# Kernel tuning notes

Measured on AMD Instinct MI355X. Metric: run time of the kernel, lower is better.

Reference implementation:

```python
import jax, jax.numpy as jnp
import numpy as np

N, L, D, PD, H, C, NP = 4, 512, 128, 64, 8, 32, 8  # batch, len, node_dim, pair_dim, heads, hidden, points
INF = 1e5
EPS = 1e-5


def _ln(x, g, b):
    m = jnp.mean(x, -1, keepdims=True)
    v = jnp.mean((x - m) ** 2, -1, keepdims=True)
    return (x - m) * jax.lax.rsqrt(v + EPS) * g + b


def _local_to_global(R, t, p):
    # p: (N,L,...,3); global = R @ p + t
    out = jnp.einsum('nlij,nl...j->nl...i', R, p)
    t_b = t.reshape(t.shape[0], t.shape[1], *([1] * (p.ndim - 3)), 3)
    return out + t_b


def _global_to_local(R, t, q):
    # local = R^T @ (q - t)
    t_b = t.reshape(t.shape[0], t.shape[1], *([1] * (q.ndim - 3)), 3)
    return jnp.einsum('nlij,nl...i->nl...j', R, q - t_b)


def _alpha_from_logits(logits, mask):
    # logits (N,L,L,H), mask (N,L,L) bool over key dim
    m = mask[..., None]
    lg = jnp.where(m, logits, logits - INF)
    a = jax.nn.softmax(lg, axis=2)
    return jnp.where(m, a, jnp.zeros_like(a))


def setup_inputs() -> dict:
    key = jax.random.key(0)
    ks = jax.random.split(key, 24)
    s = 0.02
    inp = {
        'R': jax.random.normal(ks[0], (N, L, 3, 3), jnp.float32),
        't': jax.random.normal(ks[1], (N, L, 3), jnp.float32),
        'x': jax.random.normal(ks[2], (N, L, D), jnp.float32),
        'z': jax.random.normal(ks[3], (N, L, L, PD), jnp.float32),
        'intra_mask': jax.random.bernoulli(ks[4], 0.5, (N, L, L)),
        'inter_mask': jax.random.bernoulli(ks[5], 0.5, (N, L, L)),
        'Wq': jax.random.normal(ks[6], (D, H * C), jnp.float32) * s,
        'Wk': jax.random.normal(ks[7], (D, H * C), jnp.float32) * s,
        'Wv': jax.random.normal(ks[8], (D, H * C), jnp.float32) * s,
        'Wpair': jax.random.normal(ks[9], (PD, H), jnp.float32) * s,
        'spatial_coef': jnp.full((1, 1, 1, H), np.log(np.exp(1.0) - 1.0), jnp.float32),
        'Wqp': jax.random.normal(ks[10], (D, NP * H * 3), jnp.float32) * s,
        'Wkp': jax.random.normal(ks[11], (D, NP * H * 3), jnp.float32) * s,
        'Wvp': jax.random.normal(ks[12], (D, NP * H * 3), jnp.float32) * s,
        'W1': jax.random.normal(ks[13], (H * PD + H * C + H * NP, D), jnp.float32) * s,
        'b1': jnp.zeros((D,), jnp.float32),
        'W2a': jax.random.normal(ks[14], (D, D), jnp.float32) * s,
        'b2a': jnp.zeros((D,), jnp.float32),
        'W2b': jax.random.normal(ks[15], (D, D), jnp.float32) * s,
        'b2b': jnp.zeros((D,), jnp.float32),
        'W2c': jax.random.normal(ks[16], (D, D), jnp.float32) * s,
        'b2c': jnp.zeros((D,), jnp.float32),
        'ln1_g': jnp.ones((D,), jnp.float32),
        'ln1_b': jnp.zeros((D,), jnp.float32),
        'ln2_g': jnp.ones((D,), jnp.float32),
        'ln2_b': jnp.zeros((D,), jnp.float32),
    }
    return inp


def _forward(R, t, x, z, intra_mask, inter_mask, Wq, Wk, Wv, Wpair, spatial_coef,
             Wqp, Wkp, Wvp, W1, b1, W2a, b2a, W2b, b2b, W2c, b2c,
             ln1_g, ln1_b, ln2_g, ln2_b):
    # ---- attention logits ----
    qn = (x @ Wq).reshape(N, L, H, C)
    kn = (x @ Wk).reshape(N, L, H, C)
    logits_node = jnp.einsum('nlhc,nmhc->nlmh', qn, kn) * (1.0 / np.sqrt(C))
    logits_pair = z @ Wpair  # (N,L,L,H)
    qp = _local_to_global(R, t, (x @ Wqp).reshape(N, L, H * NP, 3)).reshape(N, L, H, NP * 3)
    kp = _local_to_global(R, t, (x @ Wkp).reshape(N, L, H * NP, 3)).reshape(N, L, H, NP * 3)
    # ||q-k||^2 expanded to avoid (N,L,L,H,3P) intermediate
    sum_sq = ((qp ** 2).sum(-1)[:, :, None, :]
              + ((kp ** 2).sum(-1))[:, None, :, :]
              - 2.0 * jnp.einsum('nlhc,nmhc->nlmh', qp, kp))
    gamma = jax.nn.softplus(spatial_coef)  # (1,1,1,H)
    logits_spatial = sum_sq * (-gamma * np.sqrt(2.0 / (9.0 * NP)) / 2.0)
    logits = (logits_node + logits_pair + logits_spatial) * np.sqrt(1.0 / 3.0)

    # ---- dual-mask softmax blend ----
    intra_s = intra_mask.sum((-1, -2)).astype(jnp.float32)
    inter_s = inter_mask.sum((-1, -2)).astype(jnp.float32)
    ratio = (intra_s / (intra_s + inter_s))[:, None, None, None]
    alpha = (_alpha_from_logits(logits, intra_mask) * ratio
             + _alpha_from_logits(logits, inter_mask) * (1.0 - ratio))

    # ---- 3-stream aggregation ----
    vn = (x @ Wv).reshape(N, L, H, C)
    feat_node = jnp.einsum('nlmh,nmhc->nlhc', alpha, vn).reshape(N, L, H * C)
    feat_pair = jnp.einsum('nlmh,nlmp->nlhp', alpha, z).reshape(N, L, H * PD)
    vp = _local_to_global(R, t, (x @ Wvp).reshape(N, L, H * NP, 3)).reshape(N, L, H, NP, 3)
    fs = jnp.einsum('nlmh,nmhpc->nlhpc', alpha, vp)  # (N,L,H,P,3)
    fs = _global_to_local(R, t, fs)
    feat_spatial = jnp.linalg.norm(fs, axis=-1).reshape(N, L, H * NP)
    agg = jnp.concatenate([feat_node, feat_pair, feat_spatial], axis=-1)

    # ---- transitions ----
    feats = _ln(x + agg @ W1 + b1, ln1_g, ln1_b)
    h = jax.nn.relu(feats @ W2a + b2a)
    h = jax.nn.relu(h @ W2b + b2b)
    out = h @ W2c + b2c
    # codebook_head == 1 -> residual branch
    return _ln(feats + out, ln2_g, ln2_b)


def reference(R, t, x, z, intra_mask, inter_mask, Wq, Wk, Wv, Wpair, spatial_coef,
              Wqp, Wkp, Wvp, W1, b1, W2a, b2a, W2b, b2b, W2c, b2c,
              ln1_g, ln1_b, ln2_g, ln2_b):
    return _forward(R, t, x, z, intra_mask, inter_mask, Wq, Wk, Wv, Wpair, spatial_coef,
                    Wqp, Wkp, Wvp, W1, b1, W2a, b2a, W2b, b2b, W2c, b2c,
                    ln1_g, ln1_b, ln2_g, ln2_b)
```

## Files before the change

### kernel.cpp

```cpp
#include <hip/hip_runtime.h>
#include <math.h>

constexpr int kN = 4, kL = 512, kD = 128, kPD = 64, kH = 8, kC = 32, kNP = 8;

constexpr long OFF_FLAG = 0;
constexpr long OFF_RATIO = 16;
constexpr long OFF_SUMS = 24;
constexpr long OFF_QN  = 32;
constexpr long OFF_KN  = OFF_QN  + (long)kN * kL * 256;
constexpr long OFF_VN  = OFF_KN  + (long)kN * kL * 256;
constexpr long OFF_QP  = OFF_VN  + (long)kN * kL * 256;
constexpr long OFF_KP  = OFF_QP  + (long)kN * kL * 192;
constexpr long OFF_VP  = OFF_KP  + (long)kN * kL * 192;
constexpr long OFF_QP2 = OFF_VP  + (long)kN * kL * 192;
constexpr long OFF_KP2 = OFF_QP2 + (long)kN * kL * 8;
constexpr long OFF_AGG = OFF_KP2 + (long)kN * kL * 8;

__device__ __forceinline__ bool mask_at(const void* p, long idx, int mt) {
  if (mt == 0) return ((const unsigned char*)p)[idx] != 0;
  if (mt == 1) return ((const int*)p)[idx] != 0;
  return ((const float*)p)[idx] != 0.0f;
}

__global__ __launch_bounds__(256) void detect_mask_type_kernel(
    const unsigned int* __restrict__ m, int* __restrict__ flag) {
  __shared__ int sFloat, sGt1;
  if (threadIdx.x == 0) { sFloat = 0; sGt1 = 0; }
  __syncthreads();
  int isFloat = 0, gt1 = 0;
#pragma unroll
  for (int i = 0; i < 4; ++i) {
    const unsigned int w = m[threadIdx.x + i * 256];
    if (w == 0x3F800000u) isFloat = 1;
    if (w > 1u) gt1 = 1;
  }
  if (isFloat) atomicOr(&sFloat, 1);
  if (gt1) atomicOr(&sGt1, 1);
  __syncthreads();
  if (threadIdx.x == 0) {
    *flag = sFloat ? 2 : (sGt1 ? 0 : 1);
  }
}

__global__ void zero_sums_kernel(float* __restrict__ sums) {
  if (threadIdx.x < 8) sums[threadIdx.x] = 0.f;
}

__global__ __launch_bounds__(256) void mask_ratio_partial_kernel(
    const void* __restrict__ intra, const void* __restrict__ inter,
    const int* __restrict__ flag, float* __restrict__ sums) {
  __shared__ float red[2][256];
  const int tid = threadIdx.x;
  const int bid = blockIdx.x;
  const int n = bid >> 6;
  const int mt = *flag;
  const long base = (long)n * kL * kL + (long)(bid & 63) * 4096;
  float si = 0.f, st = 0.f;
  for (int i = tid; i < 4096; i += 256) {
    si += mask_at(intra, base + i, mt) ? 1.f : 0.f;
    st += mask_at(inter, base + i, mt) ? 1.f : 0.f;
  }
  red[0][tid] = si; red[1][tid] = st;
  __syncthreads();
  for (int s = 128; s > 0; s >>= 1) {
    if (tid < s) { red[0][tid] += red[0][tid + s]; red[1][tid] += red[1][tid + s]; }
    __syncthreads();
  }
  if (tid == 0) {
    atomicAdd(&sums[n * 2 + 0], red[0][0]);
    atomicAdd(&sums[n * 2 + 1], red[1][0]);
  }
}

__global__ void mask_ratio_final_kernel(const float* __restrict__ sums,
                                        float* __restrict__ ratio) {
  const int n = threadIdx.x;
  if (n < kN) ratio[n] = sums[n * 2] / (sums[n * 2] + sums[n * 2 + 1]);
}

__global__ __launch_bounds__(256) void proj_kernel(
    const float* __restrict__ x, const float* __restrict__ R,
    const float* __restrict__ t,
    const float* __restrict__ Wq, const float* __restrict__ Wk,
    const float* __restrict__ Wv, const float* __restrict__ Wqp,
    const float* __restrict__ Wkp, const float* __restrict__ Wvp,
    float* __restrict__ qn, float* __restrict__ kn, float* __restrict__ vn,
    float* __restrict__ qp, float* __restrict__ kp, float* __restrict__ vp,
    float* __restrict__ qp2, float* __restrict__ kp2) {
  __shared__ float xs[8][128];
  __shared__ float plocal[8][192];
  __shared__ float pglob[8][192];
  __shared__ float Rl[8][9];
  __shared__ float tl[8][3];
  const int tid = threadIdx.x;
  const int bid = blockIdx.x;
  const int n = bid >> 6;
  const int l0 = (bid & 63) * 8;
  const long rowbase = (long)n * kL + l0;

  for (int f = tid * 4; f < 8 * 128; f += 256 * 4) {
    const float4 v = *(const float4*)&x[rowbase * 128 + f];
    *(float4*)&xs[f >> 7][f & 127] = v;
  }
  if (tid < 72) Rl[tid / 9][tid % 9] = R[rowbase * 9 + tid];
  if (tid >= 72 && tid < 96) { int q = tid - 72; tl[q / 3][q % 3] = t[rowbase * 3 + q]; }
  __syncthreads();

  {
    const float* Ws[3] = {Wq, Wk, Wv};
    float* Os[3] = {qn, kn, vn};
    for (int wmat = 0; wmat < 3; ++wmat) {
      const float* W = Ws[wmat];
      float acc[8];
#pragma unroll
      for (int r = 0; r < 8; ++r) acc[r] = 0.f;
      for (int k = 0; k < 128; ++k) {
        const float w = W[k * 256 + tid];
#pragma unroll
        for (int r = 0; r < 8; ++r) acc[r] = fmaf(xs[r][k], w, acc[r]);
      }
#pragma unroll
      for (int r = 0; r < 8; ++r) Os[wmat][(rowbase + r) * 256 + tid] = acc[r];
    }
  }

  {
    const float* Ws[3] = {Wqp, Wkp, Wvp};
    float* Os[3] = {qp, kp, vp};
    float* O2s[2] = {qp2, kp2};
    for (int wmat = 0; wmat < 3; ++wmat) {
      __syncthreads();
      if (tid < 192) {
        const float* W = Ws[wmat];
        float acc[8];
#pragma unroll
        for (int r = 0; r < 8; ++r) acc[r] = 0.f;
        for (int k = 0; k < 128; ++k) {
          const float w = W[k * 192 + tid];
#pragma unroll
          for (int r = 0; r < 8; ++r) acc[r] = fmaf(xs[r][k], w, acc[r]);
        }
#pragma unroll
        for (int r = 0; r < 8; ++r) plocal[r][tid] = acc[r];
      }
      __syncthreads();
      for (int task = tid; task < 512; task += 256) {
        const int r = task >> 6, hp = task & 63;
        const float px = plocal[r][hp * 3 + 0];
        const float py = plocal[r][hp * 3 + 1];
        const float pz = plocal[r][hp * 3 + 2];
#pragma unroll
        for (int i = 0; i < 3; ++i) {
          const float g = Rl[r][i * 3 + 0] * px + Rl[r][i * 3 + 1] * py +
                          Rl[r][i * 3 + 2] * pz + tl[r][i];
          pglob[r][hp * 3 + i] = g;
          Os[wmat][(rowbase + r) * 192 + hp * 3 + i] = g;
        }
      }
      __syncthreads();
      if (wmat < 2 && tid < 64) {
        const int r = tid >> 3, h = tid & 7;
        float s = 0.f;
#pragma unroll
        for (int j = 0; j < 24; ++j) {
          const float v = pglob[r][h * 24 + j];
          s = fmaf(v, v, s);
        }
        O2s[wmat][(rowbase + r) * 8 + h] = s;
      }
    }
  }
}

__global__ __launch_bounds__(256) void attn_kernel(
    const float* __restrict__ z, const void* __restrict__ intra,
    const void* __restrict__ inter, const int* __restrict__ flag,
    const float* __restrict__ ratio_arr,
    const float* __restrict__ R, const float* __restrict__ t,
    const float* __restrict__ qn, const float* __restrict__ kn,
    const float* __restrict__ vn, const float* __restrict__ qp,
    const float* __restrict__ kp, const float* __restrict__ vp,
    const float* __restrict__ qp2, const float* __restrict__ kp2,
    const float* __restrict__ Wpair, const float* __restrict__ spatial_coef,
    float* __restrict__ agg) {
  __shared__ float lg[512][8];
  __shared__ float zbuf[64][68];
  __shared__ float mI[512], mT[512];
  __shared__ float qn_l[8][36];
  __shared__ float qp_l[192];
  __shared__ float wp[64][8];
  __shared__ float red[2][256];
  __shared__ float smax[2][8], rmul[2][8];
  __shared__ float qp2_l[8], coef_l[8];
  __shared__ float fsbuf[192];
  __shared__ float Rl[9], tl[3];

  const int tid = threadIdx.x;
  const int bid = blockIdx.x;
  const int n = bid >> 9, l = bid & 511;
  const long row = (long)n * kL + l;
  const long nbase = (long)n * kL;
  const int mt = *flag;
  const float ratio = ratio_arr[n];

  qn_l[tid >> 5][tid & 31] = qn[row * 256 + tid];
  if (tid < 192) qp_l[tid] = qp[row * 192 + tid];
  if (tid < 8) {
    qp2_l[tid] = qp2[row * 8 + tid];
    const float g = logf(1.f + expf(spatial_coef[tid]));
    coef_l[tid] = -g * sqrtf(2.f / (9.f * kNP)) * 0.5f;
  }
  for (int i = tid; i < 512; i += 256) wp[i >> 3][i & 7] = Wpair[i];
  if (tid < 9) Rl[tid] = R[row * 9 + tid];
  if (tid >= 16 && tid < 19) tl[tid - 16] = t[row * 3 + (tid - 16)];
  {
    const long mbase = row * kL;
    for (int m = tid; m < 512; m += 256) {
      mI[m] = mask_at(intra, mbase + m, mt) ? 1.f : 0.f;
      mT[m] = mask_at(inter, mbase + m, mt) ? 1.f : 0.f;
    }
  }
  __syncthreads();

  const float invsC = 0.17677669529663687f;
  const float invs3 = 0.5773502691896258f;
  const int h = tid & 7, m0 = tid >> 3;
  const float coef = coef_l[h];
  const float q2h = qp2_l[h];

  for (int mc = 0; mc < 8; ++mc) {
    __syncthreads();
    {
      const float* zrow = z + (row * kL + mc * 64) * 64;
      for (int f = tid * 4; f < 4096; f += 1024)
        *(float4*)&zbuf[f >> 6][f & 63] = *(const float4*)&zrow[f];
    }
    __syncthreads();
#pragma unroll
    for (int half = 0; half < 2; ++half) {
      const int mm = m0 + half * 32;
      const int mg = mc * 64 + mm;
      float dn = 0.f;
      const float* knp = &kn[(nbase + mg) * 256 + h * 32];
#pragma unroll
      for (int c4 = 0; c4 < 8; ++c4) {
        const float4 kv = *(const float4*)&knp[c4 * 4];
        dn = fmaf(qn_l[h][c4 * 4 + 0], kv.x, dn);
        dn = fmaf(qn_l[h][c4 * 4 + 1], kv.y, dn);
        dn = fmaf(qn_l[h][c4 * 4 + 2], kv.z, dn);
        dn = fmaf(qn_l[h][c4 * 4 + 3], kv.w, dn);
      }
      float dp = 0.f;
#pragma unroll 16
      for (int p = 0; p < 64; ++p) dp = fmaf(wp[p][h], zbuf[mm][p], dp);
      float ds = 0.f;
      const float* kpp = &kp[(nbase + mg) * 192 + h * 24];
      const float* qpp = &qp_l[h * 24];
#pragma unroll
      for (int j4 = 0; j4 < 6; ++j4) {
        const float4 kv = *(const float4*)&kpp[j4 * 4];
        ds = fmaf(qpp[j4 * 4 + 0], kv.x, ds);
        ds = fmaf(qpp[j4 * 4 + 1], kv.y, ds);
        ds = fmaf(qpp[j4 * 4 + 2], kv.z, ds);
        ds = fmaf(qpp[j4 * 4 + 3], kv.w, ds);
      }
      const float sumsq = q2h + kp2[(nbase + mg) * 8 + h] - 2.f * ds;
      lg[mg][h] = (dn * invsC + dp + sumsq * coef) * invs3;
    }
  }
  __syncthreads();

  const int h2 = tid & 7, j = tid >> 3;
  float mxI = -3.0e38f, mxT = -3.0e38f;
  for (int m = j; m < 512; m += 32) {
    const float v = lg[m][h2];
    if (mI[m] != 0.f && v > mxI) mxI = v;
    if (mT[m] != 0.f && v > mxT) mxT = v;
  }
  red[0][tid] = mxI; red[1][tid] = mxT;
  __syncthreads();
  for (int s = 16; s > 0; s >>= 1) {
    if (j < s) {
      red[0][tid] = fmaxf(red[0][tid], red[0][tid + s * 8]);
      red[1][tid] = fmaxf(red[1][tid], red[1][tid + s * 8]);
    }
    __syncthreads();
  }
  if (tid < 8) { smax[0][tid] = red[0][tid]; smax[1][tid] = red[1][tid]; }
  __syncthreads();
  const float mxIh = smax[0][h2], mxTh = smax[1][h2];
  float suI = 0.f, suT = 0.f;
  for (int m = j; m < 512; m += 32) {
    const float v = lg[m][h2];
    if (mI[m] != 0.f) suI += expf(v - mxIh);
    if (mT[m] != 0.f) suT += expf(v - mxTh);
  }
  red[0][tid] = suI; red[1][tid] = suT;
  __syncthreads();
  for (int s = 16; s > 0; s >>= 1) {
    if (j < s) {
      red[0][tid] += red[0][tid + s * 8];
      red[1][tid] += red[1][tid + s * 8];
    }
    __syncthreads();
  }
  if (tid < 8) {
    rmul[0][tid] = ratio / red[0][tid];
    rmul[1][tid] = (1.f - ratio) / red[1][tid];
  }
  __syncthreads();
  for (int idx = tid; idx < 4096; idx += 256) {
    const int m = idx >> 3, hh = idx & 7;
    const float v = lg[m][hh];
    float a = 0.f;
    if (mI[m] != 0.f) a = expf(v - smax[0][hh]) * rmul[0][hh];
    if (mT[m] != 0.f) a += expf(v - smax[1][hh]) * rmul[1][hh];
    lg[m][hh] = a;
  }
  __syncthreads();

  const int hn = tid >> 5;
  const int po = tid * 2;
  const int hpair = po >> 6, pp = po & 63;
  const int hs = tid / 24;
  float accN = 0.f, accP0 = 0.f, accP1 = 0.f, accS = 0.f;
  for (int mc = 0; mc < 8; ++mc) {
    __syncthreads();
    {
      const float* zrow = z + (row * kL + mc * 64) * 64;
      for (int f = tid * 4; f < 4096; f += 1024)
        *(float4*)&zbuf[f >> 6][f & 63] = *(const float4*)&zrow[f];
    }
    __syncthreads();
#pragma unroll 4
    for (int mm = 0; mm < 64; ++mm) {
      const int mg = mc * 64 + mm;
      const float aN = lg[mg][hn];
      accN = fmaf(aN, vn[(nbase + mg) * 256 + tid], accN);
      const float aP = lg[mg][hpair];
      accP0 = fmaf(aP, zbuf[mm][pp], accP0);
      accP1 = fmaf(aP, zbuf[mm][pp + 1], accP1);
      if (tid < 192) accS = fmaf(lg[mg][hs], vp[(nbase + mg) * 192 + tid], accS);
    }
  }
  float* aggrow = &agg[row * 832];
  aggrow[tid] = accN;
  aggrow[256 + po] = accP0;
  aggrow[256 + po + 1] = accP1;
  if (tid < 192) fsbuf[tid] = accS;
  __syncthreads();
  if (tid < 64) {
    const float gx = fsbuf[tid * 3 + 0] - tl[0];
    const float gy = fsbuf[tid * 3 + 1] - tl[1];
    const float gz = fsbuf[tid * 3 + 2] - tl[2];
    float s = 0.f;
#pragma unroll
    for (int jj = 0; jj < 3; ++jj) {
      const float lv = Rl[0 + jj] * gx + Rl[3 + jj] * gy + Rl[6 + jj] * gz;
      s = fmaf(lv, lv, s);
    }
    aggrow[768 + tid] = sqrtf(s);
  }
}

__device__ __forceinline__ float blk_sum128(float v, float* red, int tid) {
  red[tid] = v; __syncthreads();
  for (int s = 64; s > 0; s >>= 1) {
    if (tid < s) red[tid] += red[tid + s];
    __syncthreads();
  }
  const float r = red[0];
  __syncthreads();
  return r;
}

__global__ __launch_bounds__(128) void trans_kernel(
    const float* __restrict__ xg, const float* __restrict__ agg,
    const float* __restrict__ W1, const float* __restrict__ b1,
    const float* __restrict__ W2a, const float* __restrict__ b2a,
    const float* __restrict__ W2b, const float* __restrict__ b2b,
    const float* __restrict__ W2c, const float* __restrict__ b2c,
    const float* __restrict__ g1, const float* __restrict__ bb1,
    const float* __restrict__ g2, const float* __restrict__ bb2,
    float* __restrict__ out) {
  __shared__ float aggb[832];
  __shared__ float featb[128], hb1[128], hb2[128];
  __shared__ float red[128];
  const int tid = threadIdx.x;
  const long row = blockIdx.x;
  const float* arow = &agg[row * 832];
  for (int i = tid; i < 832; i += 128) aggb[i] = arow[i];
  __syncthreads();
  float acc = b1[tid];
  for (int a = 0; a < 832; ++a) acc = fmaf(aggb[a], W1[a * 128 + tid], acc);
  acc += xg[row * 128 + tid];
  const float mean = blk_sum128(acc, red, tid) * (1.f / 128.f);
  const float dv = acc - mean;
  const float var = blk_sum128(dv * dv, red, tid) * (1.f / 128.f);
  const float f = dv * rsqrtf(var + 1e-5f) * g1[tid] + bb1[tid];
  featb[tid] = f;
  __syncthreads();
  float a1 = b2a[tid];
  for (int k = 0; k < 128; ++k) a1 = fmaf(featb[k], W2a[k * 128 + tid], a1);
  hb1[tid] = fmaxf(a1, 0.f);
  __syncthreads();
  float a2 = b2b[tid];
  for (int k = 0; k < 128; ++k) a2 = fmaf(hb1[k], W2b[k * 128 + tid], a2);
  hb2[tid] = fmaxf(a2, 0.f);
  __syncthreads();
  float a3 = b2c[tid];
  for (int k = 0; k < 128; ++k) a3 = fmaf(hb2[k], W2c[k * 128 + tid], a3);
  const float res = f + a3;
  const float mean2 = blk_sum128(res, red, tid) * (1.f / 128.f);
  const float dv2 = res - mean2;
  const float var2 = blk_sum128(dv2 * dv2, red, tid) * (1.f / 128.f);
  out[row * 128 + tid] = dv2 * rsqrtf(var2 + 1e-5f) * g2[tid] + bb2[tid];
}

extern "C" void kernel_launch(void* const* d_in, const int* in_sizes, int n_in,
                              void* d_out, int out_size, void* d_ws, size_t ws_size,
                              hipStream_t stream) {
  const float* R     = (const float*)d_in[0];
  const float* t     = (const float*)d_in[1];
  const float* x     = (const float*)d_in[2];
  const float* z     = (const float*)d_in[3];
  const void*  intra = d_in[4];
  const void*  inter = d_in[5];
  const float* Wq    = (const float*)d_in[6];
  const float* Wk    = (const float*)d_in[7];
  const float* Wv    = (const float*)d_in[8];
  const float* Wpair = (const float*)d_in[9];
  const float* sc    = (const float*)d_in[10];
  const float* Wqp   = (const float*)d_in[11];
  const float* Wkp   = (const float*)d_in[12];
  const float* Wvp   = (const float*)d_in[13];
  const float* W1    = (const float*)d_in[14];
  const float* b1    = (const float*)d_in[15];
  const float* W2a   = (const float*)d_in[16];
  const float* b2a   = (const float*)d_in[17];
  const float* W2b   = (const float*)d_in[18];
  const float* b2b   = (const float*)d_in[19];
  const float* W2c   = (const float*)d_in[20];
  const float* b2c   = (const float*)d_in[21];
  const float* ln1g  = (const float*)d_in[22];
  const float* ln1b  = (const float*)d_in[23];
  const float* ln2g  = (const float*)d_in[24];
  const float* ln2b  = (const float*)d_in[25];
  float* ws = (float*)d_ws;
  float* out = (float*)d_out;

  int* flag = (int*)ws;
  float* ratio = ws + OFF_RATIO;
  float* sums = ws + OFF_SUMS;
  float* qn = ws + OFF_QN;  float* kn = ws + OFF_KN;  float* vn = ws + OFF_VN;
  float* qp = ws + OFF_QP;  float* kp = ws + OFF_KP;  float* vp = ws + OFF_VP;
  float* qp2 = ws + OFF_QP2; float* kp2 = ws + OFF_KP2;
  float* agg = ws + OFF_AGG;

  detect_mask_type_kernel<<<1, 256, 0, stream>>>((const unsigned int*)intra, flag);
  zero_sums_kernel<<<1, 64, 0, stream>>>(sums);
  mask_ratio_partial_kernel<<<256, 256, 0, stream>>>(intra, inter, flag, sums);
  mask_ratio_final_kernel<<<1, 64, 0, stream>>>(sums, ratio);
  proj_kernel<<<kN * kL / 8, 256, 0, stream>>>(x, R, t, Wq, Wk, Wv, Wqp, Wkp, Wvp,
                                               qn, kn, vn, qp, kp, vp, qp2, kp2);
  attn_kernel<<<kN * kL, 256, 0, stream>>>(z, intra, inter, flag, ratio, R, t,
                                           qn, kn, vn, qp, kp, vp, qp2, kp2,
                                           Wpair, sc, agg);
  trans_kernel<<<kN * kL, 128, 0, stream>>>(x, agg, W1, b1, W2a, b2a, W2b, b2b,
                                            W2c, b2c, ln1g, ln1b, ln2g, ln2b, out);
}
```

Baseline: 1.205 ms.

## Precompute pair bias in separate kernel and fuse online softmax with aggregation

A new zw_kernel computes z @ Wpair for every pair once, so the attention kernel reads a precomputed bias instead of staging z in shared memory for the logits. The attention kernel then switches to a single-pass online softmax: per 64-key chunk it computes logits, updates running maxima and denominators for both masks, rescales the accumulators, and immediately accumulates node, pair and spatial features with float4 register tiling. Partial sums are reduced across waves through shared scratch at the end. This replaces the second z read and the multi-pass softmax, at the cost of an extra kernel that reads all of z, a small zw buffer, and higher register pressure.

```diff
diff --git a/kernel.cpp b/kernel.cpp
--- a/kernel.cpp
+++ b/kernel.cpp
@@ -15,6 +15,9 @@
 constexpr long OFF_QP2 = OFF_VP  + (long)kN * kL * 192;
 constexpr long OFF_KP2 = OFF_QP2 + (long)kN * kL * 8;
 constexpr long OFF_AGG = OFF_KP2 + (long)kN * kL * 8;
+constexpr long OFF_ZW  = OFF_AGG + (long)kN * kL * 832;
+
+#define E4(v,kk) ((kk)==0?(v).x:((kk)==1?(v).y:((kk)==2?(v).z:(v).w)))
 
 __device__ __forceinline__ bool mask_at(const void* p, long idx, int mt) {
   if (mt == 0) return ((const unsigned char*)p)[idx] != 0;
@@ -37,9 +40,7 @@
   if (isFloat) atomicOr(&sFloat, 1);
   if (gt1) atomicOr(&sGt1, 1);
   __syncthreads();
-  if (threadIdx.x == 0) {
-    *flag = sFloat ? 2 : (sGt1 ? 0 : 1);
-  }
+  if (threadIdx.x == 0) *flag = sFloat ? 2 : (sGt1 ? 0 : 1);
 }
 
 __global__ void zero_sums_kernel(float* __restrict__ sums) {
@@ -172,6 +173,59 @@
   }
 }
 
+__global__ __launch_bounds__(256) void zw_kernel(
+    const float* __restrict__ z, const float* __restrict__ Wp,
+    float* __restrict__ zw) {
+  const int tid = threadIdx.x;
+  const int r = tid >> 3, pseg = tid & 7;
+  float w[8][8];
+#pragma unroll
+  for (int pp = 0; pp < 8; ++pp) {
+    const float4 wa = *(const float4*)&Wp[(pseg * 8 + pp) * 8];
+    const float4 wb = *(const float4*)&Wp[(pseg * 8 + pp) * 8 + 4];
+    w[pp][0] = wa.x; w[pp][1] = wa.y; w[pp][2] = wa.z; w[pp][3] = wa.w;
+    w[pp][4] = wb.x; w[pp][5] = wb.y; w[pp][6] = wb.z; w[pp][7] = wb.w;
+  }
+  const long base = (long)blockIdx.x * 512;
+  for (int it = 0; it < 16; ++it) {
+    const long row = base + it * 32 + r;
+    const float* zr = &z[row * 64 + pseg * 8];
+    const float4 za = *(const float4*)zr;
+    const float4 zb = *(const float4*)(zr + 4);
+    float a[8];
+#pragma unroll
+    for (int hh = 0; hh < 8; ++hh) {
+      float s = za.x * w[0][hh];
+      s = fmaf(za.y, w[1][hh], s);
+      s = fmaf(za.z, w[2][hh], s);
+      s = fmaf(za.w, w[3][hh], s);
+      s = fmaf(zb.x, w[4][hh], s);
+      s = fmaf(zb.y, w[5][hh], s);
+      s = fmaf(zb.z, w[6][hh], s);
+      s = fmaf(zb.w, w[7][hh], s);
+      a[hh] = s;
+    }
+    float b[4];
+#pragma unroll
+    for (int j = 0; j < 4; ++j) {
+      const float t0 = __shfl_xor(a[j], 4, 64);
+      const float t1 = __shfl_xor(a[j + 4], 4, 64);
+      b[j] = (pseg & 4) ? (a[j + 4] + t1) : (a[j] + t0);
+    }
+    float c2[2];
+#pragma unroll
+    for (int j = 0; j < 2; ++j) {
+      const float t0 = __shfl_xor(b[j], 2, 64);
+      const float t1 = __shfl_xor(b[j + 2], 2, 64);
+      c2[j] = (pseg & 2) ? (b[j + 2] + t1) : (b[j] + t0);
+    }
+    const float t0 = __shfl_xor(c2[0], 1, 64);
+    const float t1 = __shfl_xor(c2[1], 1, 64);
+    const float res = (pseg & 1) ? (c2[1] + t1) : (c2[0] + t0);
+    zw[row * 8 + pseg] = res;
+  }
+}
+
 __global__ __launch_bounds__(256) void attn_kernel(
     const float* __restrict__ z, const void* __restrict__ intra,
     const void* __restrict__ inter, const int* __restrict__ flag,
@@ -181,36 +235,41 @@
     const float* __restrict__ vn, const float* __restrict__ qp,
     const float* __restrict__ kp, const float* __restrict__ vp,
     const float* __restrict__ qp2, const float* __restrict__ kp2,
-    const float* __restrict__ Wpair, const float* __restrict__ spatial_coef,
+    const float* __restrict__ zw, const float* __restrict__ spatial_coef,
     float* __restrict__ agg) {
-  __shared__ float lg[512][8];
-  __shared__ float zbuf[64][68];
+  __shared__ float qn_l[8][36];
+  __shared__ float qp_l[8][28];
   __shared__ float mI[512], mT[512];
-  __shared__ float qn_l[8][36];
-  __shared__ float qp_l[192];
-  __shared__ float wp[64][8];
-  __shared__ float red[2][256];
-  __shared__ float smax[2][8], rmul[2][8];
+  __shared__ float lgEh[2][8][72];
+  __shared__ float wredM[2][4][8], wredD[2][4][8];
+  __shared__ float MxS[2][8], fac[2][8], Sden[2][8], wfin[2][8];
   __shared__ float qp2_l[8], coef_l[8];
+  __shared__ float scratch[2048];
   __shared__ float fsbuf[192];
   __shared__ float Rl[9], tl[3];
 
   const int tid = threadIdx.x;
-  const int bid = blockIdx.x;
-  const int n = bid >> 9, l = bid & 511;
-  const long row = (long)n * kL + l;
+  const long row = blockIdx.x;
+  const int n = blockIdx.x >> 9;
   const long nbase = (long)n * kL;
   const int mt = *flag;
   const float ratio = ratio_arr[n];
+  const int lane = tid & 63, wv = tid >> 6;
+  const int h = tid & 7, m0 = tid >> 3;
+
+  const int offN = tid >> 6, c64 = tid & 63, h_n = c64 >> 3;
+  const int offP = tid >> 5, hg = (tid >> 4) & 1, p4 = tid & 15;
+  const int offS = tid / 48, ps = tid - offS * 48, h_s = ps / 6;
 
   qn_l[tid >> 5][tid & 31] = qn[row * 256 + tid];
-  if (tid < 192) qp_l[tid] = qp[row * 192 + tid];
+  if (tid < 192) qp_l[tid / 24][tid % 24] = qp[row * 192 + tid];
   if (tid < 8) {
     qp2_l[tid] = qp2[row * 8 + tid];
     const float g = logf(1.f + expf(spatial_coef[tid]));
     coef_l[tid] = -g * sqrtf(2.f / (9.f * kNP)) * 0.5f;
   }
-  for (int i = tid; i < 512; i += 256) wp[i >> 3][i & 7] = Wpair[i];
+  if (tid < 16) { MxS[tid >> 3][tid & 7] = -3.0e38f; Sden[tid >> 3][tid & 7] = 0.f; }
+  if (tid < 64) ((float*)wredD)[tid] = 0.f;
   if (tid < 9) Rl[tid] = R[row * 9 + tid];
   if (tid >= 16 && tid < 19) tl[tid - 16] = t[row * 3 + (tid - 16)];
   {
@@ -224,130 +283,250 @@
 
   const float invsC = 0.17677669529663687f;
   const float invs3 = 0.5773502691896258f;
-  const int h = tid & 7, m0 = tid >> 3;
-  const float coef = coef_l[h];
   const float q2h = qp2_l[h];
-
-  for (int mc = 0; mc < 8; ++mc) {
+  const float coefh = coef_l[h];
+
+  float4 zero4 = {0.f, 0.f, 0.f, 0.f};
+  float4 accN[2] = {zero4, zero4};
+  float4 accS[2] = {zero4, zero4};
+  float4 accP[2][4];
+#pragma unroll
+  for (int s = 0; s < 2; ++s)
+#pragma unroll
+    for (int j = 0; j < 4; ++j) accP[s][j] = zero4;
+
+  for (int c = 0; c < 8; ++c) {
+    const int mgb = c * 64;
+    float vhalf[2]; bool bI[2], bT[2];
+    float mxI = -3.0e38f, mxT = -3.0e38f;
+#pragma unroll
+    for (int half = 0; half < 2; ++half) {
+      const int mm = m0 + 32 * half;
+      const int mg = mgb + mm;
+      const long krow = nbase + mg;
+      float dn = 0.f;
+      const float4* knp = (const float4*)&kn[krow * 256 + h * 32];
+      const float4* qnp = (const float4*)&qn_l[h][0];
+#pragma unroll
+      for (int c4 = 0; c4 < 8; ++c4) {
+        const float4 kv = knp[c4]; const float4 qv = qnp[c4];
+        dn = fmaf(qv.x, kv.x, dn); dn = fmaf(qv.y, kv.y, dn);
+        dn = fmaf(qv.z, kv.z, dn); dn = fmaf(qv.w, kv.w, dn);
+      }
+      float ds = 0.f;
+      const float4* kpp = (const float4*)&kp[krow * 192 + h * 24];
+      const float4* qpp = (const float4*)&qp_l[h][0];
+#pragma unroll
+      for (int j4 = 0; j4 < 6; ++j4) {
+        const float4 kv = kpp[j4]; const float4 qv = qpp[j4];
+        ds = fmaf(qv.x, kv.x, ds); ds = fmaf(qv.y, kv.y, ds);
+        ds = fmaf(qv.z, kv.z, ds); ds = fmaf(qv.w, kv.w, ds);
+      }
+      const float dp = zw[((row << 9) + mg) * 8 + h];
+      const float sumsq = q2h + kp2[krow * 8 + h] - 2.f * ds;
+      const float v = (dn * invsC + dp + sumsq * coefh) * invs3;
+      vhalf[half] = v;
+      const bool mi = (mI[mg] != 0.f), mtt = (mT[mg] != 0.f);
+      bI[half] = mi; bT[half] = mtt;
+      if (mi) mxI = fmaxf(mxI, v);
+      if (mtt) mxT = fmaxf(mxT, v);
+    }
+#pragma unroll
+    for (int d = 8; d <= 32; d <<= 1) {
+      mxI = fmaxf(mxI, __shfl_xor(mxI, d, 64));
+      mxT = fmaxf(mxT, __shfl_xor(mxT, d, 64));
+    }
+    if (lane < 8) { wredM[0][wv][lane] = mxI; wredM[1][wv][lane] = mxT; }
+    __syncthreads();
+    if (tid < 16) {
+      const int s = tid >> 3, hh = tid & 7;
+      const float cm = fmaxf(fmaxf(wredM[s][0][hh], wredM[s][1][hh]),
+                             fmaxf(wredM[s][2][hh], wredM[s][3][hh]));
+      const float old = MxS[s][hh];
+      const float nm = fmaxf(old, cm);
+      const float f = __expf(old - nm);
+      const float dsum = wredD[s][0][hh] + wredD[s][1][hh] +
+                         wredD[s][2][hh] + wredD[s][3][hh];
+      Sden[s][hh] = (Sden[s][hh] + dsum) * f;
+      MxS[s][hh] = nm; fac[s][hh] = f;
+    }
     __syncthreads();
     {
-      const float* zrow = z + (row * kL + mc * 64) * 64;
-      for (int f = tid * 4; f < 4096; f += 1024)
-        *(float4*)&zbuf[f >> 6][f & 63] = *(const float4*)&zrow[f];
-    }
-    __syncthreads();
-#pragma unroll
-    for (int half = 0; half < 2; ++half) {
-      const int mm = m0 + half * 32;
-      const int mg = mc * 64 + mm;
-      float dn = 0.f;
-      const float* knp = &kn[(nbase + mg) * 256 + h * 32];
-#pragma unroll
-      for (int c4 = 0; c4 < 8; ++c4) {
-        const float4 kv = *(const float4*)&knp[c4 * 4];
-        dn = fmaf(qn_l[h][c4 * 4 + 0], kv.x, dn);
-        dn = fmaf(qn_l[h][c4 * 4 + 1], kv.y, dn);
-        dn = fmaf(qn_l[h][c4 * 4 + 2], kv.z, dn);
-        dn = fmaf(qn_l[h][c4 * 4 + 3], kv.w, dn);
-      }
-      float dp = 0.f;
-#pragma unroll 16
-      for (int p = 0; p < 64; ++p) dp = fmaf(wp[p][h], zbuf[mm][p], dp);
-      float ds = 0.f;
-      const float* kpp = &kp[(nbase + mg) * 192 + h * 24];
-      const float* qpp = &qp_l[h * 24];
-#pragma unroll
-      for (int j4 = 0; j4 < 6; ++j4) {
-        const float4 kv = *(const float4*)&kpp[j4 * 4];
-        ds = fmaf(qpp[j4 * 4 + 0], kv.x, ds);
-        ds = fmaf(qpp[j4 * 4 + 1], kv.y, ds);
-        ds = fmaf(qpp[j4 * 4 + 2], kv.z, ds);
-        ds = fmaf(qpp[j4 * 4 + 3], kv.w, ds);
-      }
-      const float sumsq = q2h + kp2[(nbase + mg) * 8 + h] - 2.f * ds;
-      lg[mg][h] = (dn * invsC + dp + sumsq * coef) * invs3;
-    }
-  }
-  __syncthreads();
-
-  const int h2 = tid & 7, j = tid >> 3;
-  float mxI = -3.0e38f, mxT = -3.0e38f;
-  for (int m = j; m < 512; m += 32) {
-    const float v = lg[m][h2];
-    if (mI[m] != 0.f && v > mxI) mxI = v;
-    if (mT[m] != 0.f && v > mxT) mxT = v;
-  }
-  red[0][tid] = mxI; red[1][tid] = mxT;
-  __syncthreads();
-  for (int s = 16; s > 0; s >>= 1) {
-    if (j < s) {
-      red[0][tid] = fmaxf(red[0][tid], red[0][tid + s * 8]);
-      red[1][tid] = fmaxf(red[1][tid], red[1][tid + s * 8]);
-    }
-    __syncthreads();
-  }
-  if (tid < 8) { smax[0][tid] = red[0][tid]; smax[1][tid] = red[1][tid]; }
-  __syncthreads();
-  const float mxIh = smax[0][h2], mxTh = smax[1][h2];
-  float suI = 0.f, suT = 0.f;
-  for (int m = j; m < 512; m += 32) {
-    const float v = lg[m][h2];
-    if (mI[m] != 0.f) suI += expf(v - mxIh);
-    if (mT[m] != 0.f) suT += expf(v - mxTh);
-  }
-  red[0][tid] = suI; red[1][tid] = suT;
-  __syncthreads();
-  for (int s = 16; s > 0; s >>= 1) {
-    if (j < s) {
-      red[0][tid] += red[0][tid + s * 8];
-      red[1][tid] += red[1][tid + s * 8];
-    }
-    __syncthreads();
-  }
-  if (tid < 8) {
-    rmul[0][tid] = ratio / red[0][tid];
-    rmul[1][tid] = (1.f - ratio) / red[1][tid];
-  }
-  __syncthreads();
-  for (int idx = tid; idx < 4096; idx += 256) {
-    const int m = idx >> 3, hh = idx & 7;
-    const float v = lg[m][hh];
-    float a = 0.f;
-    if (mI[m] != 0.f) a = expf(v - smax[0][hh]) * rmul[0][hh];
-    if (mT[m] != 0.f) a += expf(v - smax[1][hh]) * rmul[1][hh];
-    lg[m][hh] = a;
-  }
-  __syncthreads();
-
-  const int hn = tid >> 5;
-  const int po = tid * 2;
-  const int hpair = po >> 6, pp = po & 63;
-  const int hs = tid / 24;
-  float accN = 0.f, accP0 = 0.f, accP1 = 0.f, accS = 0.f;
-  for (int mc = 0; mc < 8; ++mc) {
+      const float fnI = fac[0][h_n], fnT = fac[1][h_n];
+      accN[0].x *= fnI; accN[0].y *= fnI; accN[0].z *= fnI; accN[0].w *= fnI;
+      accN[1].x *= fnT; accN[1].y *= fnT; accN[1].z *= fnT; accN[1].w *= fnT;
+      const float fsI = fac[0][h_s], fsT = fac[1][h_s];
+      accS[0].x *= fsI; accS[0].y *= fsI; accS[0].z *= fsI; accS[0].w *= fsI;
+      accS[1].x *= fsT; accS[1].y *= fsT; accS[1].z *= fsT; accS[1].w *= fsT;
+#pragma unroll
+      for (int j = 0; j < 4; ++j) {
+        const float fpI = fac[0][hg * 4 + j], fpT = fac[1][hg * 4 + j];
+        accP[0][j].x *= fpI; accP[0][j].y *= fpI; accP[0][j].z *= fpI; accP[0][j].w *= fpI;
+        accP[1][j].x *= fpT; accP[1][j].y *= fpT; accP[1][j].z *= fpT; accP[1][j].w *= fpT;
+      }
+    }
+    {
+      float dI = 0.f, dT = 0.f;
+      const float MxIh = MxS[0][h], MxTh = MxS[1][h];
+#pragma unroll
+      for (int half = 0; half < 2; ++half) {
+        const int mm = m0 + 32 * half;
+        const float eI = bI[half] ? __expf(vhalf[half] - MxIh) : 0.f;
+        const float eT = bT[half] ? __expf(vhalf[half] - MxTh) : 0.f;
+        lgEh[0][h][mm] = eI; lgEh[1][h][mm] = eT;
+        dI += eI; dT += eT;
+      }
+#pragma unroll
+      for (int d = 8; d <= 32; d <<= 1) {
+        dI += __shfl_xor(dI, d, 64);
+        dT += __shfl_xor(dT, d, 64);
+      }
+      if (lane < 8) { wredD[0][wv][lane] = dI; wredD[1][wv][lane] = dT; }
+    }
     __syncthreads();
     {
-      const float* zrow = z + (row * kL + mc * 64) * 64;
-      for (int f = tid * 4; f < 4096; f += 1024)
-        *(float4*)&zbuf[f >> 6][f & 63] = *(const float4*)&zrow[f];
-    }
-    __syncthreads();
-#pragma unroll 4
-    for (int mm = 0; mm < 64; ++mm) {
-      const int mg = mc * 64 + mm;
-      const float aN = lg[mg][hn];
-      accN = fmaf(aN, vn[(nbase + mg) * 256 + tid], accN);
-      const float aP = lg[mg][hpair];
-      accP0 = fmaf(aP, zbuf[mm][pp], accP0);
-      accP1 = fmaf(aP, zbuf[mm][pp + 1], accP1);
-      if (tid < 192) accS = fmaf(lg[mg][hs], vp[(nbase + mg) * 192 + tid], accS);
-    }
-  }
+      const long vbase = (nbase + mgb + offN * 16) * 256 + c64 * 4;
+#pragma unroll
+      for (int q = 0; q < 4; ++q) {
+        const float4 eIq = *(const float4*)&lgEh[0][h_n][offN * 16 + q * 4];
+        const float4 eTq = *(const float4*)&lgEh[1][h_n][offN * 16 + q * 4];
+#define NODE_STEP(kk)                                                        \
+        {                                                                    \
+          const float4 v4 = *(const float4*)&vn[vbase + (q * 4 + kk) * 256]; \
+          const float ei = E4(eIq, kk), et = E4(eTq, kk);                    \
+          accN[0].x = fmaf(ei, v4.x, accN[0].x);                             \
+          accN[0].y = fmaf(ei, v4.y, accN[0].y);                             \
+          accN[0].z = fmaf(ei, v4.z, accN[0].z);                             \
+          accN[0].w = fmaf(ei, v4.w, accN[0].w);                             \
+          accN[1].x = fmaf(et, v4.x, accN[1].x);                             \
+          accN[1].y = fmaf(et, v4.y, accN[1].y);                             \
+          accN[1].z = fmaf(et, v4.z, accN[1].z);                             \
+          accN[1].w = fmaf(et, v4.w, accN[1].w);                             \
+        }
+        NODE_STEP(0) NODE_STEP(1) NODE_STEP(2) NODE_STEP(3)
+#undef NODE_STEP
+      }
+    }
+    {
+      const long zbase = (row * kL + mgb + offP * 8) * 64 + p4 * 4;
+#pragma unroll
+      for (int half4 = 0; half4 < 2; ++half4) {
+        const int mmb = offP * 8 + half4 * 4;
+        float4 eIr[4], eTr[4];
+#pragma unroll
+        for (int j = 0; j < 4; ++j) {
+          eIr[j] = *(const float4*)&lgEh[0][hg * 4 + j][mmb];
+          eTr[j] = *(const float4*)&lgEh[1][hg * 4 + j][mmb];
+        }
+#define PAIR_STEP(kk)                                                         \
+        {                                                                     \
+          const float4 z4 = *(const float4*)&z[zbase + (half4 * 4 + kk) * 64];\
+          _Pragma("unroll")                                                   \
+          for (int j = 0; j < 4; ++j) {                                       \
+            const float ei = E4(eIr[j], kk), et = E4(eTr[j], kk);             \
+            accP[0][j].x = fmaf(ei, z4.x, accP[0][j].x);                      \
+            accP[0][j].y = fmaf(ei, z4.y, accP[0][j].y);                      \
+            accP[0][j].z = fmaf(ei, z4.z, accP[0][j].z);                      \
+            accP[0][j].w = fmaf(ei, z4.w, accP[0][j].w);                      \
+            accP[1][j].x = fmaf(et, z4.x, accP[1][j].x);                      \
+            accP[1][j].y = fmaf(et, z4.y, accP[1][j].y);                      \
+            accP[1][j].z = fmaf(et, z4.z, accP[1][j].z);                      \
+            accP[1][j].w = fmaf(et, z4.w, accP[1][j].w);                      \
+          }                                                                   \
+        }
+        PAIR_STEP(0) PAIR_STEP(1) PAIR_STEP(2) PAIR_STEP(3)
+#undef PAIR_STEP
+      }
+    }
+    if (tid < 192) {
+      const long pbase = (nbase + mgb + offS * 16) * 192 + ps * 4;
+#pragma unroll
+      for (int q = 0; q < 4; ++q) {
+        const float4 eIq = *(const float4*)&lgEh[0][h_s][offS * 16 + q * 4];
+        const float4 eTq = *(const float4*)&lgEh[1][h_s][offS * 16 + q * 4];
+#define SPAT_STEP(kk)                                                        \
+        {                                                                    \
+          const float4 v4 = *(const float4*)&vp[pbase + (q * 4 + kk) * 192]; \
+          const float ei = E4(eIq, kk), et = E4(eTq, kk);                    \
+          accS[0].x = fmaf(ei, v4.x, accS[0].x);                             \
+          accS[0].y = fmaf(ei, v4.y, accS[0].y);                             \
+          accS[0].z = fmaf(ei, v4.z, accS[0].z);                             \
+          accS[0].w = fmaf(ei, v4.w, accS[0].w);                             \
+          accS[1].x = fmaf(et, v4.x, accS[1].x);                             \
+          accS[1].y = fmaf(et, v4.y, accS[1].y);                             \
+          accS[1].z = fmaf(et, v4.z, accS[1].z);                             \
+          accS[1].w = fmaf(et, v4.w, accS[1].w);                             \
+        }
+        SPAT_STEP(0) SPAT_STEP(1) SPAT_STEP(2) SPAT_STEP(3)
+#undef SPAT_STEP
+      }
+    }
+  }
+
+  if (tid < 16) {
+    const int s = tid >> 3, hh = tid & 7;
+    const float S = Sden[s][hh] + wredD[s][0][hh] + wredD[s][1][hh] +
+                    wredD[s][2][hh] + wredD[s][3][hh];
+    const float wsc = (s == 0) ? ratio : (1.f - ratio);
+    wfin[s][hh] = (S > 0.f) ? (wsc / S) : 0.f;
+  }
+  __syncthreads();
+
   float* aggrow = &agg[row * 832];
-  aggrow[tid] = accN;
-  aggrow[256 + po] = accP0;
-  aggrow[256 + po + 1] = accP1;
-  if (tid < 192) fsbuf[tid] = accS;
+  *(float4*)&scratch[(offN * 2 + 0) * 256 + c64 * 4] = accN[0];
+  *(float4*)&scratch[(offN * 2 + 1) * 256 + c64 * 4] = accN[1];
+  __syncthreads();
+  {
+    const int col = tid, hh = col >> 5;
+    const float FI = scratch[col] + scratch[512 + col] + scratch[1024 + col] + scratch[1536 + col];
+    const float FT = scratch[256 + col] + scratch[768 + col] + scratch[1280 + col] + scratch[1792 + col];
+    aggrow[col] = wfin[0][hh] * FI + wfin[1][hh] * FT;
+  }
+  __syncthreads();
+#pragma unroll
+  for (int s = 0; s < 2; ++s)
+#pragma unroll
+    for (int j = 0; j < 4; ++j) {
+      float4 v = accP[s][j];
+      v.x += __shfl_xor(v.x, 32, 64); v.y += __shfl_xor(v.y, 32, 64);
+      v.z += __shfl_xor(v.z, 32, 64); v.w += __shfl_xor(v.w, 32, 64);
+      accP[s][j] = v;
+    }
+  float FI0 = 0.f, FI1 = 0.f, FT0 = 0.f, FT1 = 0.f;
+  if ((tid & 32) == 0) {
+#pragma unroll
+    for (int j = 0; j < 4; ++j)
+      *(float4*)&scratch[wv * 512 + (hg * 4 + j) * 64 + p4 * 4] = accP[0][j];
+  }
+  __syncthreads();
+  FI0 = scratch[tid] + scratch[512 + tid] + scratch[1024 + tid] + scratch[1536 + tid];
+  FI1 = scratch[256 + tid] + scratch[768 + tid] + scratch[1280 + tid] + scratch[1792 + tid];
+  __syncthreads();
+  if ((tid & 32) == 0) {
+#pragma unroll
+    for (int j = 0; j < 4; ++j)
+      *(float4*)&scratch[wv * 512 + (hg * 4 + j) * 64 + p4 * 4] = accP[1][j];
+  }
+  __syncthreads();
+  FT0 = scratch[tid] + scratch[512 + tid] + scratch[1024 + tid] + scratch[1536 + tid];
+  FT1 = scratch[256 + tid] + scratch[768 + tid] + scratch[1280 + tid] + scratch[1792 + tid];
+  {
+    const int h0 = tid >> 6, h1 = (tid + 256) >> 6;
+    aggrow[256 + tid] = wfin[0][h0] * FI0 + wfin[1][h0] * FT0;
+    aggrow[512 + tid] = wfin[0][h1] * FI1 + wfin[1][h1] * FT1;
+  }
+  __syncthreads();
+  if (tid < 192) {
+    *(float4*)&scratch[(offS * 2 + 0) * 192 + ps * 4] = accS[0];
+    *(float4*)&scratch[(offS * 2 + 1) * 192 + ps * 4] = accS[1];
+  }
+  __syncthreads();
+  if (tid < 192) {
+    const float FI = scratch[tid] + scratch[384 + tid] + scratch[768 + tid] + scratch[1152 + tid];
+    const float FT = scratch[192 + tid] + scratch[576 + tid] + scratch[960 + tid] + scratch[1344 + tid];
+    const int hh = tid / 24;
+    fsbuf[tid] = wfin[0][hh] * FI + wfin[1][hh] * FT;
+  }
   __syncthreads();
   if (tid < 64) {
     const float gx = fsbuf[tid * 3 + 0] - tl[0];
@@ -456,6 +635,7 @@
   float* qp = ws + OFF_QP;  float* kp = ws + OFF_KP;  float* vp = ws + OFF_VP;
   float* qp2 = ws + OFF_QP2; float* kp2 = ws + OFF_KP2;
   float* agg = ws + OFF_AGG;
+  float* zw  = ws + OFF_ZW;
 
   detect_mask_type_kernel<<<1, 256, 0, stream>>>((const unsigned int*)intra, flag);
   zero_sums_kernel<<<1, 64, 0, stream>>>(sums);
@@ -463,9 +643,10 @@
   mask_ratio_final_kernel<<<1, 64, 0, stream>>>(sums, ratio);
   proj_kernel<<<kN * kL / 8, 256, 0, stream>>>(x, R, t, Wq, Wk, Wv, Wqp, Wkp, Wvp,
                                                qn, kn, vn, qp, kp, vp, qp2, kp2);
+  zw_kernel<<<2048, 256, 0, stream>>>(z, Wpair, zw);
   attn_kernel<<<kN * kL, 256, 0, stream>>>(z, intra, inter, flag, ratio, R, t,
                                            qn, kn, vn, qp, kp, vp, qp2, kp2,
-                                           Wpair, sc, agg);
+                                           zw, sc, agg);
   trans_kernel<<<kN * kL, 128, 0, stream>>>(x, agg, W1, b1, W2a, b2a, W2b, b2b,
                                             W2c, b2c, ln1g, ln1b, ln2g, ln2b, out);
 }
```

Result: faster. 1.104 ms (-8.4%).
